# Kernel tuning notes

Hardware: AMD Instinct MI355X
Metric: run time of the kernel (lower is better)

The kernel has to match this reference:

```python
import jax, jax.numpy as jnp
import numpy as np

EMBED_DIM = 1024
NUM_HEADS = 16
HEAD_DIM = EMBED_DIM // NUM_HEADS
B, T = 4, 2048


def setup_inputs() -> dict:
    key = jax.random.key(0)
    ks = jax.random.split(key, 5)
    s = 1.0 / np.sqrt(EMBED_DIM)
    x = jax.random.normal(ks[0], (B, T, EMBED_DIM), dtype=jnp.float32)
    W_qkv = jax.random.uniform(ks[1], (EMBED_DIM, 3 * EMBED_DIM), minval=-s, maxval=s, dtype=jnp.float32)
    b_qkv = jax.random.uniform(ks[2], (3 * EMBED_DIM,), minval=-s, maxval=s, dtype=jnp.float32)
    W_proj = jax.random.uniform(ks[3], (EMBED_DIM, EMBED_DIM), minval=-s, maxval=s, dtype=jnp.float32)
    b_proj = jax.random.uniform(ks[4], (EMBED_DIM,), minval=-s, maxval=s, dtype=jnp.float32)
    return {"x": x, "W_qkv": W_qkv, "b_qkv": b_qkv, "W_proj": W_proj, "b_proj": b_proj}


def reference(x, W_qkv, b_qkv, W_proj, b_proj):
    Bq, Tq, C = x.shape
    H, D = NUM_HEADS, HEAD_DIM
    qkv = x @ W_qkv + b_qkv                      # [B,T,3C]
    qkv = qkv.reshape(Bq, Tq, 3, H, D)
    q = qkv[:, :, 0].transpose(0, 2, 1, 3)       # [B,H,T,D]
    k = qkv[:, :, 1].transpose(0, 2, 1, 3)
    v = qkv[:, :, 2].transpose(0, 2, 1, 3)
    scale = 1.0 / jnp.sqrt(jnp.asarray(D, x.dtype))
    attn = jnp.einsum('bhqd,bhkd->bhqk', q, k) * scale  # [B,H,T,T]
    mask = jnp.tril(jnp.ones((Tq, Tq), dtype=bool))     # causal: keep lower triangle
    attn = jnp.where(mask, attn, jnp.asarray(-jnp.inf, attn.dtype))
    attn = jax.nn.softmax(attn, axis=-1)
    out = jnp.einsum('bhqk,bhkd->bhqd', attn, v)        # [B,H,T,D]
    out = out.transpose(0, 2, 1, 3).reshape(Bq, Tq, C)
    return out @ W_proj + b_proj
```

## Files before the change

kernel.cpp:

```cpp
#include <hip/hip_runtime.h>
#include <stdint.h>

typedef unsigned short ushort_t;
typedef __attribute__((ext_vector_type(4))) unsigned int  u32x4;
typedef __attribute__((ext_vector_type(2))) unsigned int  u32x2;
typedef __attribute__((ext_vector_type(4))) float         f32x4;
typedef __attribute__((ext_vector_type(8))) __bf16        bf16x8;
typedef __attribute__((ext_vector_type(2))) __bf16        bf16x2;

__device__ __forceinline__ ushort_t f2bf(float f) {
    unsigned int u = __float_as_uint(f);
    u += 0x7fffu + ((u >> 16) & 1u);
    return (ushort_t)(u >> 16);
}
__device__ __forceinline__ unsigned int pack2bf(float a, float b) {
    return (unsigned int)f2bf(a) | ((unsigned int)f2bf(b) << 16);
}
#if __has_builtin(__builtin_amdgcn_cvt_pk_bf16_f32)
__device__ __forceinline__ unsigned int pack2bf_fast(float a, float b) {
    bf16x2 v = __builtin_amdgcn_cvt_pk_bf16_f32(a, b);
    return __builtin_bit_cast(unsigned int, v);
}
#else
__device__ __forceinline__ unsigned int pack2bf_fast(float a, float b) {
    return pack2bf(a, b);
}
#endif
__device__ __forceinline__ f32x4 mfma16(bf16x8 a, bf16x8 b, f32x4 c) {
    return __builtin_amdgcn_mfma_f32_16x16x32_bf16(a, b, c, 0, 0, 0);
}
__device__ __forceinline__ bf16x8 ldfrag(const ushort_t* p) {
    return __builtin_bit_cast(bf16x8, *(const u32x4*)p);
}

__device__ __forceinline__ void gld16(const ushort_t* g, ushort_t* l) {
    __builtin_amdgcn_global_load_lds(
        (const __attribute__((address_space(1))) void*)g,
        (__attribute__((address_space(3))) void*)l, 16, 0, 0);
}

__device__ __forceinline__ void wg_barrier() {
    asm volatile("s_waitcnt lgkmcnt(0)\n\ts_barrier" ::: "memory");
}

#define QSCALE 0.18033688011112042f

__global__ __launch_bounds__(256) void prep(const float* __restrict__ X,
                                            ushort_t* __restrict__ Xb,
                                            const float* __restrict__ Wq,
                                            ushort_t* __restrict__ Wqt,
                                            const float* __restrict__ Wp,
                                            ushort_t* __restrict__ Wpt) {
    __shared__ float tile[32][33];
    const int tid = threadIdx.x;
    const int b   = blockIdx.x;
    if (b < 4096) {
        long i = ((long)b * 256 + tid) * 8;
        float4 a = *(const float4*)(X + i);
        float4 c = *(const float4*)(X + i + 4);
        u32x4 pk;
        pk.x = pack2bf(a.x, a.y); pk.y = pack2bf(a.z, a.w);
        pk.z = pack2bf(c.x, c.y); pk.w = pack2bf(c.z, c.w);
        *(u32x4*)(Xb + i) = pk;
        return;
    }
    const float* W; ushort_t* Wt; int N, bx, by;
    if (b < 7168) { int idx = b - 4096; W = Wq; Wt = Wqt; N = 3072; bx = idx % 96; by = idx / 96; }
    else          { int idx = b - 7168; W = Wp; Wt = Wpt; N = 1024; bx = idx & 31; by = idx >> 5; }
    const int tx = tid & 31, ty = tid >> 5;
    const int n0 = bx * 32, k0 = by * 32;
    for (int p = 0; p < 4; ++p)
        tile[ty + 8*p][tx] = W[(long)(k0 + ty + 8*p) * N + n0 + tx];
    __syncthreads();
    for (int p = 0; p < 4; ++p)
        Wt[(long)(n0 + ty + 8*p) * 1024 + k0 + tx] = f2bf(tile[tx][ty + 8*p]);
}

__global__ __launch_bounds__(256) void gemm_qkv(const ushort_t* __restrict__ Xb,
                                                const ushort_t* __restrict__ Wt,
                                                const float* __restrict__ bias,
                                                ushort_t* __restrict__ Qo,
                                                ushort_t* __restrict__ Ko,
                                                ushort_t* __restrict__ Vto) {
    __shared__ __align__(16) ushort_t smem[24576];

    const int tid  = threadIdx.x;
    const int g    = blockIdx.x;
    const int grp  = g / 192, rr = g % 192;
    const int m0   = (grp * 8 + (rr & 7)) * 128;
    const int n0   = (rr >> 3) * 128;
    const int lane = tid & 63, w = tid >> 6;
    const int quad = lane >> 4, l16 = lane & 15;
    const int wm = (w >> 1) * 64, wn = (w & 1) * 64;

    const int srow  = tid >> 2;
    const int slot  = tid & 3;
    const int oct   = slot ^ ((tid >> 3) & 3);
    const int rslot = (quad ^ ((l16 >> 1) & 3)) * 8;
    const int wbase = (tid & 192) * 8;

    const ushort_t* Ap = Xb + (long)(m0 + srow) * 1024 + oct * 8;
    const ushort_t* Bp = Wt + (long)(n0 + srow) * 1024 + oct * 8;

    f32x4 acc[4][4] = {};

    auto issue = [&](int pf, int ibuf) {
        int k = (pf < 32) ? (pf << 5) : 0;
        gld16(Ap + k,         &smem[ibuf + wbase]);
        gld16(Ap + k + 65536, &smem[ibuf + wbase + 2048]);
        gld16(Bp + k,         &smem[ibuf + wbase + 4096]);
        gld16(Bp + k + 65536, &smem[ibuf + wbase + 6144]);
    };
    auto step = [&](int p, int rbuf, int ibuf) {
        asm volatile("s_waitcnt vmcnt(4)\n\ts_barrier" ::: "memory");
        issue(p + 2, ibuf);
        const ushort_t* As = smem + rbuf;
        const ushort_t* Bs = As + 4096;
        bf16x8 af[4], bfr[4];
        for (int i = 0; i < 4; ++i)
            af[i] = ldfrag(&As[(wm + 16*i + l16) * 32 + rslot]);
        for (int j = 0; j < 4; ++j)
            bfr[j] = ldfrag(&Bs[(wn + 16*j + l16) * 32 + rslot]);
        __builtin_amdgcn_s_setprio(1);
        for (int i = 0; i < 4; ++i)
            for (int j = 0; j < 4; ++j)
                acc[i][j] = mfma16(af[i], bfr[j], acc[i][j]);
        __builtin_amdgcn_s_setprio(0);
    };

    issue(0, 0);
    issue(1, 8192);
    for (int p = 0; p < 30; p += 3) {
        step(p,     0,     16384);
        step(p + 1, 8192,  0);
        step(p + 2, 16384, 8192);
    }
    step(30, 0,    16384);
    step(31, 8192, 0);

    float bj[4];
    for (int j = 0; j < 4; ++j) bj[j] = bias[n0 + wn + 16*j + l16];
    const int bb = m0 >> 11, t0m = m0 & 2047;
    asm volatile("s_waitcnt vmcnt(0)" ::: "memory");
    __syncthreads();

    if (n0 < 2048) {
        ushort_t* dst = (n0 < 1024) ? Qo : Ko;
        const float scale = (n0 < 1024) ? QSCALE : 1.0f;
        const int nbase = (n0 < 1024) ? n0 : n0 - 1024;
        for (int i = 0; i < 4; ++i)
            for (int j = 0; j < 4; ++j) {
                int nl = wn + 16*j + l16;
                for (int r = 0; r < 4; ++r) {
                    int ml = wm + 16*i + quad*4 + r;
                    smem[ml * 136 + nl] = f2bf((acc[i][j][r] + bj[j]) * scale);
                }
            }
        __syncthreads();
        for (int c = 0; c < 8; ++c) {
            int chunk = tid + 256 * c;
            int row = chunk >> 4, nc = (chunk & 15) * 8;
            int n = nbase + nc;
            int hh = n >> 6, d = n & 63;
            *(u32x4*)&dst[((long)(bb*16 + hh) * 2048 + t0m + row) * 64 + d] =
                *(const u32x4*)&smem[row * 136 + nc];
        }
    } else {
        for (int i = 0; i < 4; ++i)
            for (int j = 0; j < 4; ++j) {
                int nl = wn + 16*j + l16;
                for (int r = 0; r < 4; ++r) {
                    int ml = wm + 16*i + quad*4 + r;
                    smem[nl * 136 + ml] = f2bf(acc[i][j][r] + bj[j]);
                }
            }
        __syncthreads();
        for (int c = 0; c < 8; ++c) {
            int chunk = tid + 256 * c;
            int row = chunk >> 4, mc = (chunk & 15) * 8;
            int n = n0 - 2048 + row;
            int hh = n >> 6, d = n & 63;
            *(u32x4*)&Vto[((long)(bb*16 + hh) * 64 + d) * 2048 + t0m + mc] =
                *(const u32x4*)&smem[row * 136 + mc];
        }
    }
}

__global__ __launch_bounds__(256) void attn_kernel(const ushort_t* __restrict__ Q,
                                                   const ushort_t* __restrict__ K,
                                                   const ushort_t* __restrict__ Vt,
                                                   ushort_t* __restrict__ O) {
    __shared__ __align__(16) ushort_t Ks[2][64 * 64];
    __shared__ __align__(16) ushort_t Vs[2][64 * 64];
    __shared__ __align__(16) ushort_t Ps[128 * 72];

    const int tid  = threadIdx.x;
    const int lane = tid & 63, w = tid >> 6, quad = lane >> 4, l16 = lane & 15;
    const int g    = blockIdx.x;
    const int bh   = (g & 7) + 8 * ((g >> 3) & 7);
    const int qt   = 15 - (g >> 6);
    const ushort_t* qptr = Q  + (long)bh * 2048 * 64;
    const ushort_t* kptr = K  + (long)bh * 2048 * 64;
    const ushort_t* vptr = Vt + (long)bh * 64 * 2048;
    const int bb2 = bh >> 4, h = bh & 15;

    const int srow = tid >> 3;
    const int slot = tid & 7;
    const int oct  = slot ^ (srow & 7);
    const int koff = srow * 64 + oct * 8;
    const int voff = srow * 2048 + oct * 8;
    const int wofs = srow * 64 + slot * 8;

    const int qbase = qt * 128;
    const int nkt = 2 * qt + 2;

    const u32x4 ones_u = {0x3F803F80u, 0x3F803F80u, 0x3F803F80u, 0x3F803F80u};
    const bf16x8 ones = __builtin_bit_cast(bf16x8, ones_u);

    for (int c = 0; c < 4; ++c) {
        int flat = tid + 256 * c;
        int row = flat >> 3, kc = (flat & 7) * 8;
        *(u32x4*)&Ps[row * 72 + kc] = *(const u32x4*)&qptr[(long)(qbase + row) * 64 + kc];
    }
    wg_barrier();
    bf16x8 qf[2][2];
    for (int nt = 0; nt < 2; ++nt)
        for (int kk = 0; kk < 2; ++kk)
            qf[nt][kk] = ldfrag(&Ps[(32*w + 16*nt + l16) * 72 + kk*32 + quad*8]);

    f32x4 acc[2][4] = {};
    f32x4 accl[2]   = {};

    auto phase = [&](int kt, ushort_t* Kb, ushort_t* Vb) {
        const int kbase = kt * 64;
        if (kbase > qbase + 32*w + 31) return;
        f32x4 s[4][2] = {};
        __builtin_amdgcn_s_setprio(1);
        for (int kk = 0; kk < 2; ++kk)
            for (int mt = 0; mt < 4; ++mt) {
                bf16x8 kf = ldfrag(&Kb[(16*mt + l16) * 64 + ((4*kk + quad) ^ (l16 & 7)) * 8]);
                for (int nt = 0; nt < 2; ++nt)
                    s[mt][nt] = mfma16(kf, qf[nt][kk], s[mt][nt]);
            }
        __builtin_amdgcn_s_setprio(0);
        if (kbase + 63 > qbase + 32*w) {
            for (int mt = 0; mt < 4; ++mt)
                for (int nt = 0; nt < 2; ++nt) {
                    int qv = qbase + 32*w + 16*nt + l16;
                    for (int r = 0; r < 4; ++r)
                        if (kbase + 16*mt + 4*quad + r > qv)
                            s[mt][nt][r] = -__builtin_inff();
                }
        }
        for (int nt = 0; nt < 2; ++nt)
            for (int mt = 0; mt < 4; ++mt) {
                float p0 = __builtin_amdgcn_exp2f(s[mt][nt][0]);
                float p1 = __builtin_amdgcn_exp2f(s[mt][nt][1]);
                float p2 = __builtin_amdgcn_exp2f(s[mt][nt][2]);
                float p3 = __builtin_amdgcn_exp2f(s[mt][nt][3]);
                u32x2 pk;
                pk.x = pack2bf_fast(p0, p1);
                pk.y = pack2bf_fast(p2, p3);
                *(u32x2*)&Ps[(32*w + 16*nt + l16) * 72 + 16*mt + 4*quad] = pk;
            }
        __builtin_amdgcn_s_setprio(1);
        for (int kk = 0; kk < 2; ++kk) {
            bf16x8 pf0 = ldfrag(&Ps[(32*w + l16) * 72 + kk*32 + quad*8]);
            bf16x8 pf1 = ldfrag(&Ps[(32*w + 16 + l16) * 72 + kk*32 + quad*8]);
            accl[0] = mfma16(pf0, ones, accl[0]);
            accl[1] = mfma16(pf1, ones, accl[1]);
            for (int jd = 0; jd < 4; ++jd) {
                bf16x8 vf = ldfrag(&Vb[(16*jd + l16) * 64 + ((4*kk + quad) ^ (l16 & 7)) * 8]);
                acc[0][jd] = mfma16(pf0, vf, acc[0][jd]);
                acc[1][jd] = mfma16(pf1, vf, acc[1][jd]);
            }
        }
        __builtin_amdgcn_s_setprio(0);
    };

    u32x4 KA0 = *(const u32x4*)(kptr + koff);
    u32x4 KA1 = *(const u32x4*)(kptr + koff + 2048);
    u32x4 VA0 = *(const u32x4*)(vptr + voff);
    u32x4 VA1 = *(const u32x4*)(vptr + voff + 65536);
    u32x4 KB0 = *(const u32x4*)(kptr + 4096 + koff);
    u32x4 KB1 = *(const u32x4*)(kptr + 4096 + koff + 2048);
    u32x4 VB0 = *(const u32x4*)(vptr + 64 + voff);
    u32x4 VB1 = *(const u32x4*)(vptr + 64 + voff + 65536);

    for (int kt = 0; kt < nkt; kt += 2) {
        {
            *(u32x4*)&Ks[0][wofs]        = KA0;
            *(u32x4*)&Ks[0][wofs + 2048] = KA1;
            *(u32x4*)&Vs[0][wofs]        = VA0;
            *(u32x4*)&Vs[0][wofs + 2048] = VA1;
            int kf = (kt + 2 < nkt) ? kt + 2 : kt;
            KA0 = *(const u32x4*)(kptr + kf*4096 + koff);
            KA1 = *(const u32x4*)(kptr + kf*4096 + koff + 2048);
            VA0 = *(const u32x4*)(vptr + kf*64 + voff);
            VA1 = *(const u32x4*)(vptr + kf*64 + voff + 65536);
            wg_barrier();
            phase(kt, Ks[0], Vs[0]);
        }
        {
            *(u32x4*)&Ks[1][wofs]        = KB0;
            *(u32x4*)&Ks[1][wofs + 2048] = KB1;
            *(u32x4*)&Vs[1][wofs]        = VB0;
            *(u32x4*)&Vs[1][wofs + 2048] = VB1;
            int kf = (kt + 3 < nkt) ? kt + 3 : kt + 1;
            KB0 = *(const u32x4*)(kptr + kf*4096 + koff);
            KB1 = *(const u32x4*)(kptr + kf*4096 + koff + 2048);
            VB0 = *(const u32x4*)(vptr + kf*64 + voff);
            VB1 = *(const u32x4*)(vptr + kf*64 + voff + 65536);
            wg_barrier();
            phase(kt + 1, Ks[1], Vs[1]);
        }
    }

    for (int i = 0; i < 2; ++i)
        for (int r = 0; r < 4; ++r) {
            float linv = 1.0f / accl[i][r];
            int t = qbase + 32*w + 16*i + 4*quad + r;
            for (int jd = 0; jd < 4; ++jd) {
                int d = 16*jd + l16;
                O[((long)(bb2*2048 + t)) * 1024 + h*64 + d] = f2bf(acc[i][jd][r] * linv);
            }
        }
}

__global__ __launch_bounds__(256) void gemm_proj(const ushort_t* __restrict__ A,
                                                 const ushort_t* __restrict__ Wt,
                                                 const float* __restrict__ bias,
                                                 float* __restrict__ Out) {
    __shared__ __align__(16) ushort_t smem[24576];

    const int tid  = threadIdx.x;
    const int g    = blockIdx.x;
    const int grp  = g / 64, rr = g % 64;
    const int m0   = (grp * 8 + (rr & 7)) * 128;
    const int n0   = (rr >> 3) * 128;
    const int lane = tid & 63, w = tid >> 6;
    const int quad = lane >> 4, l16 = lane & 15;
    const int wm = (w >> 1) * 64, wn = (w & 1) * 64;

    const int srow  = tid >> 2;
    const int slot  = tid & 3;
    const int oct   = slot ^ ((tid >> 3) & 3);
    const int rslot = (quad ^ ((l16 >> 1) & 3)) * 8;
    const int wbase = (tid & 192) * 8;

    const ushort_t* Ap = A  + (long)(m0 + srow) * 1024 + oct * 8;
    const ushort_t* Bp = Wt + (long)(n0 + srow) * 1024 + oct * 8;

    f32x4 acc[4][4] = {};

    auto issue = [&](int pf, int ibuf) {
        int k = (pf < 32) ? (pf << 5) : 0;
        gld16(Ap + k,         &smem[ibuf + wbase]);
        gld16(Ap + k + 65536, &smem[ibuf + wbase + 2048]);
        gld16(Bp + k,         &smem[ibuf + wbase + 4096]);
        gld16(Bp + k + 65536, &smem[ibuf + wbase + 6144]);
    };
    auto step = [&](int p, int rbuf, int ibuf) {
        asm volatile("s_waitcnt vmcnt(4)\n\ts_barrier" ::: "memory");
        issue(p + 2, ibuf);
        const ushort_t* As = smem + rbuf;
        const ushort_t* Bs = As + 4096;
        bf16x8 af[4], bfr[4];
        for (int i = 0; i < 4; ++i)
            af[i] = ldfrag(&As[(wm + 16*i + l16) * 32 + rslot]);
        for (int j = 0; j < 4; ++j)
            bfr[j] = ldfrag(&Bs[(wn + 16*j + l16) * 32 + rslot]);
        __builtin_amdgcn_s_setprio(1);
        for (int i = 0; i < 4; ++i)
            for (int j = 0; j < 4; ++j)
                acc[i][j] = mfma16(af[i], bfr[j], acc[i][j]);
        __builtin_amdgcn_s_setprio(0);
    };

    issue(0, 0);
    issue(1, 8192);
    for (int p = 0; p < 30; p += 3) {
        step(p,     0,     16384);
        step(p + 1, 8192,  0);
        step(p + 2, 16384, 8192);
    }
    step(30, 0,    16384);
    step(31, 8192, 0);
    asm volatile("s_waitcnt vmcnt(0)" ::: "memory");

    float bj[4];
    for (int j = 0; j < 4; ++j) bj[j] = bias[n0 + wn + 16*j + l16];
    for (int i = 0; i < 4; ++i)
        for (int j = 0; j < 4; ++j)
            for (int r = 0; r < 4; ++r) {
                int m = m0 + wm + 16*i + quad*4 + r;
                int n = n0 + wn + 16*j + l16;
                Out[(long)m * 1024 + n] = acc[i][j][r] + bj[j];
            }
}

extern "C" void kernel_launch(void* const* d_in, const int* in_sizes, int n_in,
                              void* d_out, int out_size, void* d_ws, size_t ws_size,
                              hipStream_t stream) {
    const float* x     = (const float*)d_in[0];
    const float* Wqkv  = (const float*)d_in[1];
    const float* bqkv  = (const float*)d_in[2];
    const float* Wproj = (const float*)d_in[3];
    const float* bproj = (const float*)d_in[4];
    float* out = (float*)d_out;

    ushort_t* wqkvt  = (ushort_t*)d_ws;
    ushort_t* wprojt = wqkvt  + 3072 * 1024;
    ushort_t* Qb     = wprojt + 1024 * 1024;
    ushort_t* Kb     = Qb  + 8388608;
    ushort_t* Vtb    = Kb  + 8388608;
    ushort_t* XbA2   = Vtb + 8388608;

    prep<<<8192, 256, 0, stream>>>(x, XbA2, Wqkv, wqkvt, Wproj, wprojt);
    gemm_qkv<<<1536, 256, 0, stream>>>(XbA2, wqkvt, bqkv, Qb, Kb, Vtb);
    attn_kernel<<<1024, 256, 0, stream>>>(Qb, Kb, Vtb, XbA2);
    gemm_proj<<<512, 256, 0, stream>>>(XbA2, wprojt, bproj, out);
}
```

Baseline: 240.7 us.

## Single-buffer K/V tiles and XOR-swizzle P tile to shrink attention LDS

Replaces the double-buffered K/V shared tiles and two-stage register prefetch with a single LDS buffer and a one-tile-ahead register prefetch, adding a barrier before each tile store. The padded 72-stride P/Q tile becomes an unpadded 64-stride tile with an XOR swizzle to avoid bank conflicts. This cuts LDS use and register pressure, allowing more workgroups per CU, at the cost of an extra barrier per K tile and less latency hiding between loads and compute.

```diff
diff --git a/kernel.cpp b/kernel.cpp
--- a/kernel.cpp
+++ b/kernel.cpp
@@ -190,9 +190,9 @@
                                                    const ushort_t* __restrict__ K,
                                                    const ushort_t* __restrict__ Vt,
                                                    ushort_t* __restrict__ O) {
-    __shared__ __align__(16) ushort_t Ks[2][64 * 64];
-    __shared__ __align__(16) ushort_t Vs[2][64 * 64];
-    __shared__ __align__(16) ushort_t Ps[128 * 72];
+    __shared__ __align__(16) ushort_t Ks[64 * 64];
+    __shared__ __align__(16) ushort_t Vs[64 * 64];
+    __shared__ __align__(16) ushort_t Ps[128 * 64];
 
     const int tid  = threadIdx.x;
     const int lane = tid & 63, w = tid >> 6, quad = lane >> 4, l16 = lane & 15;
@@ -220,25 +220,28 @@
     for (int c = 0; c < 4; ++c) {
         int flat = tid + 256 * c;
         int row = flat >> 3, kc = (flat & 7) * 8;
-        *(u32x4*)&Ps[row * 72 + kc] = *(const u32x4*)&qptr[(long)(qbase + row) * 64 + kc];
+        *(u32x4*)&Ps[row * 64 + (kc ^ ((row & 7) * 8))] =
+            *(const u32x4*)&qptr[(long)(qbase + row) * 64 + kc];
     }
     wg_barrier();
     bf16x8 qf[2][2];
     for (int nt = 0; nt < 2; ++nt)
-        for (int kk = 0; kk < 2; ++kk)
-            qf[nt][kk] = ldfrag(&Ps[(32*w + 16*nt + l16) * 72 + kk*32 + quad*8]);
+        for (int kk = 0; kk < 2; ++kk) {
+            int row = 32*w + 16*nt + l16;
+            qf[nt][kk] = ldfrag(&Ps[row * 64 + ((kk*32 + quad*8) ^ ((row & 7) * 8))]);
+        }
 
     f32x4 acc[2][4] = {};
     f32x4 accl[2]   = {};
 
-    auto phase = [&](int kt, ushort_t* Kb, ushort_t* Vb) {
+    auto phase = [&](int kt) {
         const int kbase = kt * 64;
         if (kbase > qbase + 32*w + 31) return;
         f32x4 s[4][2] = {};
         __builtin_amdgcn_s_setprio(1);
         for (int kk = 0; kk < 2; ++kk)
             for (int mt = 0; mt < 4; ++mt) {
-                bf16x8 kf = ldfrag(&Kb[(16*mt + l16) * 64 + ((4*kk + quad) ^ (l16 & 7)) * 8]);
+                bf16x8 kf = ldfrag(&Ks[(16*mt + l16) * 64 + ((4*kk + quad) ^ (l16 & 7)) * 8]);
                 for (int nt = 0; nt < 2; ++nt)
                     s[mt][nt] = mfma16(kf, qf[nt][kk], s[mt][nt]);
             }
@@ -252,7 +255,8 @@
                             s[mt][nt][r] = -__builtin_inff();
                 }
         }
-        for (int nt = 0; nt < 2; ++nt)
+        for (int nt = 0; nt < 2; ++nt) {
+            int row = 32*w + 16*nt + l16;
             for (int mt = 0; mt < 4; ++mt) {
                 float p0 = __builtin_amdgcn_exp2f(s[mt][nt][0]);
                 float p1 = __builtin_amdgcn_exp2f(s[mt][nt][1]);
@@ -261,16 +265,18 @@
                 u32x2 pk;
                 pk.x = pack2bf_fast(p0, p1);
                 pk.y = pack2bf_fast(p2, p3);
-                *(u32x2*)&Ps[(32*w + 16*nt + l16) * 72 + 16*mt + 4*quad] = pk;
-            }
+                *(u32x2*)&Ps[row * 64 + ((16*mt + 4*quad) ^ ((row & 7) * 8))] = pk;
+            }
+        }
         __builtin_amdgcn_s_setprio(1);
         for (int kk = 0; kk < 2; ++kk) {
-            bf16x8 pf0 = ldfrag(&Ps[(32*w + l16) * 72 + kk*32 + quad*8]);
-            bf16x8 pf1 = ldfrag(&Ps[(32*w + 16 + l16) * 72 + kk*32 + quad*8]);
+            int r0 = 32*w + l16, r1 = 32*w + 16 + l16;
+            bf16x8 pf0 = ldfrag(&Ps[r0 * 64 + ((kk*32 + quad*8) ^ ((r0 & 7) * 8))]);
+            bf16x8 pf1 = ldfrag(&Ps[r1 * 64 + ((kk*32 + quad*8) ^ ((r1 & 7) * 8))]);
             accl[0] = mfma16(pf0, ones, accl[0]);
             accl[1] = mfma16(pf1, ones, accl[1]);
             for (int jd = 0; jd < 4; ++jd) {
-                bf16x8 vf = ldfrag(&Vb[(16*jd + l16) * 64 + ((4*kk + quad) ^ (l16 & 7)) * 8]);
+                bf16x8 vf = ldfrag(&Vs[(16*jd + l16) * 64 + ((4*kk + quad) ^ (l16 & 7)) * 8]);
                 acc[0][jd] = mfma16(pf0, vf, acc[0][jd]);
                 acc[1][jd] = mfma16(pf1, vf, acc[1][jd]);
             }
@@ -278,42 +284,24 @@
         __builtin_amdgcn_s_setprio(0);
     };
 
-    u32x4 KA0 = *(const u32x4*)(kptr + koff);
-    u32x4 KA1 = *(const u32x4*)(kptr + koff + 2048);
-    u32x4 VA0 = *(const u32x4*)(vptr + voff);
-    u32x4 VA1 = *(const u32x4*)(vptr + voff + 65536);
-    u32x4 KB0 = *(const u32x4*)(kptr + 4096 + koff);
-    u32x4 KB1 = *(const u32x4*)(kptr + 4096 + koff + 2048);
-    u32x4 VB0 = *(const u32x4*)(vptr + 64 + voff);
-    u32x4 VB1 = *(const u32x4*)(vptr + 64 + voff + 65536);
-
-    for (int kt = 0; kt < nkt; kt += 2) {
-        {
-            *(u32x4*)&Ks[0][wofs]        = KA0;
-            *(u32x4*)&Ks[0][wofs + 2048] = KA1;
-            *(u32x4*)&Vs[0][wofs]        = VA0;
-            *(u32x4*)&Vs[0][wofs + 2048] = VA1;
-            int kf = (kt + 2 < nkt) ? kt + 2 : kt;
-            KA0 = *(const u32x4*)(kptr + kf*4096 + koff);
-            KA1 = *(const u32x4*)(kptr + kf*4096 + koff + 2048);
-            VA0 = *(const u32x4*)(vptr + kf*64 + voff);
-            VA1 = *(const u32x4*)(vptr + kf*64 + voff + 65536);
-            wg_barrier();
-            phase(kt, Ks[0], Vs[0]);
-        }
-        {
-            *(u32x4*)&Ks[1][wofs]        = KB0;
-            *(u32x4*)&Ks[1][wofs + 2048] = KB1;
-            *(u32x4*)&Vs[1][wofs]        = VB0;
-            *(u32x4*)&Vs[1][wofs + 2048] = VB1;
-            int kf = (kt + 3 < nkt) ? kt + 3 : kt + 1;
-            KB0 = *(const u32x4*)(kptr + kf*4096 + koff);
-            KB1 = *(const u32x4*)(kptr + kf*4096 + koff + 2048);
-            VB0 = *(const u32x4*)(vptr + kf*64 + voff);
-            VB1 = *(const u32x4*)(vptr + kf*64 + voff + 65536);
-            wg_barrier();
-            phase(kt + 1, Ks[1], Vs[1]);
-        }
+    u32x4 K0 = *(const u32x4*)(kptr + koff);
+    u32x4 K1 = *(const u32x4*)(kptr + koff + 2048);
+    u32x4 V0 = *(const u32x4*)(vptr + voff);
+    u32x4 V1 = *(const u32x4*)(vptr + voff + 65536);
+
+    for (int kt = 0; kt < nkt; ++kt) {
+        wg_barrier();
+        *(u32x4*)&Ks[wofs]        = K0;
+        *(u32x4*)&Ks[wofs + 2048] = K1;
+        *(u32x4*)&Vs[wofs]        = V0;
+        *(u32x4*)&Vs[wofs + 2048] = V1;
+        int kf = (kt + 1 < nkt) ? kt + 1 : kt;
+        K0 = *(const u32x4*)(kptr + kf*4096 + koff);
+        K1 = *(const u32x4*)(kptr + kf*4096 + koff + 2048);
+        V0 = *(const u32x4*)(vptr + kf*64 + voff);
+        V1 = *(const u32x4*)(vptr + kf*64 + voff + 65536);
+        wg_barrier();
+        phase(kt);
     }
 
     for (int i = 0; i < 2; ++i)
```

After: 265.9 us. 10.5% more time.
